# Optimization experiments

Hardware: AMD Instinct MI355X
Metric: run time of the kernel (lower is better)

## Reference

```python
import jax, jax.numpy as jnp
import numpy as np

EMB = 1024
HEADS = 16
HEAD_DIM = EMB // HEADS


def setup_inputs() -> dict:
    key = jax.random.key(0)
    ks = jax.random.split(key, 9)
    s = 1.0 / np.sqrt(EMB)
    x = jax.random.normal(ks[0], (2, 2048, EMB), dtype=jnp.float32)
    Wq = jax.random.normal(ks[1], (EMB, EMB), dtype=jnp.float32) * s
    bq = jnp.zeros((EMB,), dtype=jnp.float32)
    Wk = jax.random.normal(ks[2], (EMB, EMB), dtype=jnp.float32) * s
    bk = jnp.zeros((EMB,), dtype=jnp.float32)
    Wv = jax.random.normal(ks[3], (EMB, EMB), dtype=jnp.float32) * s
    bv = jnp.zeros((EMB,), dtype=jnp.float32)
    Wo = jax.random.normal(ks[4], (EMB, EMB), dtype=jnp.float32) * s
    bo = jnp.zeros((EMB,), dtype=jnp.float32)
    return {"x": x, "Wq": Wq, "bq": bq, "Wk": Wk, "bk": bk,
            "Wv": Wv, "bv": bv, "Wo": Wo, "bo": bo}


def reference(x, Wq, bq, Wk, bk, Wv, bv, Wo, bo):
    B, S, E = x.shape
    # torch Linear: y = x @ W.T + b
    q = x @ Wq.T + bq
    k = x @ Wk.T + bk
    v = x @ Wv.T + bv
    # [B,S,E] -> [B,H,S,D]
    q = q.reshape(B, S, HEADS, HEAD_DIM).transpose(0, 2, 1, 3)
    k = k.reshape(B, S, HEADS, HEAD_DIM).transpose(0, 2, 1, 3)
    v = v.reshape(B, S, HEADS, HEAD_DIM).transpose(0, 2, 1, 3)
    energy = jnp.einsum('bhqd,bhkd->bhqk', q, k)
    scaling = jnp.float32(E) ** 0.5  # NOTE: sqrt(emb_size), not sqrt(head_dim), as in source
    att = jax.nn.softmax(energy / scaling, axis=-1)
    out = jnp.einsum('bhqk,bhkd->bhqd', att, v)
    out = out.transpose(0, 2, 1, 3).reshape(B, S, E)
    return out @ Wo.T + bo
```

## Files before the change

### kernel.cpp

```cpp
#include <hip/hip_runtime.h>
#include <stdint.h>


typedef _Float16 half8  __attribute__((ext_vector_type(8)));
typedef _Float16 half4v __attribute__((ext_vector_type(4)));
typedef float    f32x4  __attribute__((ext_vector_type(4)));
typedef float    f32x16 __attribute__((ext_vector_type(16)));

#define GLD16(g, l) __builtin_amdgcn_global_load_lds(                         \
    (__attribute__((address_space(1))) void*)(g),                            \
    (__attribute__((address_space(3))) void*)(l), 16, 0, 0)

#define MFMA16(a, b, c) __builtin_amdgcn_mfma_f32_16x16x32_f16((a), (b), (c), 0, 0, 0)
#define MFMA32(a, b, c) __builtin_amdgcn_mfma_f32_32x32x16_f16((a), (b), (c), 0, 0, 0)

#if __has_builtin(__builtin_amdgcn_exp2f)
#define EXP2(x) __builtin_amdgcn_exp2f(x)
#else
#define EXP2(x) exp2f(x)
#endif

static __device__ inline uint32_t pk_u32(float a, float b)
{
    auto t = __builtin_amdgcn_cvt_pkrtz(a, b);
    return __builtin_bit_cast(uint32_t, t);
}

__global__ void cvt_all(const float* __restrict__ x,  const float* __restrict__ wq,
                        const float* __restrict__ wk, const float* __restrict__ wv,
                        const float* __restrict__ wo, _Float16* __restrict__ xb,
                        _Float16* __restrict__ wqkv, _Float16* __restrict__ wob)
{
    int i = blockIdx.x * blockDim.x + threadIdx.x;
    const float* src; _Float16* dst; int off;
    if (i < 1048576)      { src = x;  dst = xb;                 off = i; }
    else if (i < 1310720) { src = wq; dst = wqkv;               off = i - 1048576; }
    else if (i < 1572864) { src = wk; dst = wqkv + 1048576;     off = i - 1310720; }
    else if (i < 1835008) { src = wv; dst = wqkv + 2097152;     off = i - 1572864; }
    else                  { src = wo; dst = wob;                off = i - 1835008; }
    float4 f = ((const float4*)src)[off];
    half4v h = { (_Float16)f.x, (_Float16)f.y, (_Float16)f.z, (_Float16)f.w };
    ((half4v*)dst)[off] = h;
}

template<int BN, int MODE>
__global__ __launch_bounds__(256, MODE == 0 ? 3 : 2)
void gemm_f16(const _Float16* __restrict__ A, const _Float16* __restrict__ W,
              const float* __restrict__ b0, const float* __restrict__ b1,
              const float* __restrict__ b2, _Float16* __restrict__ o0,
              _Float16* __restrict__ o1, _Float16* __restrict__ o2,
              float* __restrict__ outf, float qscale)
{
    constexpr int NI = BN / 32;
    __shared__ _Float16 lA[128 * 64];
    __shared__ _Float16 lB[BN * 64];
    const int m0 = blockIdx.y * 128, n0 = blockIdx.x * BN;
    const int tid = threadIdx.x, lane = tid & 63, w = tid >> 6;
    const int wr = (w >> 1) * 64, wc = (w & 1) * (BN / 2);
    const int lrow = lane & 15, lk4 = lane >> 4;
    f32x4 acc[4][NI] = {};

    for (int k0 = 0; k0 < 1024; k0 += 64) {
        __syncthreads();
#pragma unroll
        for (int c = 0; c < 4; ++c) {
            int sidx = c * 256 + tid;
            int row = sidx >> 3, sl = sidx & 7;
            int gc = k0 + ((sl ^ (row & 7)) << 3);
            GLD16(A + (size_t)(m0 + row) * 1024 + gc, lA + (size_t)(c * 256 + w * 64) * 8);
        }
#pragma unroll
        for (int c = 0; c < BN / 32; ++c) {
            int sidx = c * 256 + tid;
            int row = sidx >> 3, sl = sidx & 7;
            int gc = k0 + ((sl ^ (row & 7)) << 3);
            GLD16(W + (size_t)(n0 + row) * 1024 + gc, lB + (size_t)(c * 256 + w * 64) * 8);
        }
        __syncthreads();

#pragma unroll
        for (int kd = 0; kd < 2; ++kd) {
            half8 af[4], bf[NI];
#pragma unroll
            for (int mi = 0; mi < 4; ++mi) {
                int ra = wr + mi * 16 + lrow;
                af[mi] = *(const half8*)(lA + ra * 64 + (((kd * 4 + lk4) ^ (ra & 7)) * 8));
            }
#pragma unroll
            for (int ni = 0; ni < NI; ++ni) {
                int rb = wc + ni * 16 + lrow;
                bf[ni] = *(const half8*)(lB + rb * 64 + (((kd * 4 + lk4) ^ (rb & 7)) * 8));
            }
#pragma unroll
            for (int mi = 0; mi < 4; ++mi)
#pragma unroll
                for (int ni = 0; ni < NI; ++ni)
                    acc[mi][ni] = MFMA16(af[mi], bf[ni], acc[mi][ni]);
        }
    }

    if (MODE == 0) {
        const int which = n0 >> 10;
        const float* bp = which == 0 ? b0 : which == 1 ? b1 : b2;
        const float scale = which == 0 ? qscale : 1.f;
        const int nh = n0 & 1023;
        float bcol[NI];
#pragma unroll
        for (int ni = 0; ni < NI; ++ni) bcol[ni] = bp[nh + wc + ni * 16 + lrow];
        if (which == 2) {
#pragma unroll
            for (int mi = 0; mi < 4; ++mi)
#pragma unroll
                for (int ni = 0; ni < NI; ++ni) {
                    int cg = nh + wc + ni * 16 + lrow;
                    int hh = cg >> 6, dd = cg & 63;
                    int sb = m0 + wr + mi * 16 + lk4 * 4;
                    int bb = sb >> 11, ss = sb & 2047;
                    int tile = ss >> 6, ks = (ss >> 4) & 3;
                    int hb = (ss >> 3) & 1, j0 = ss & 7;
                    int c2 = dd >> 5, l31v = dd & 31;
                    half4v pkv;
#pragma unroll
                    for (int r = 0; r < 4; ++r)
                        pkv[r] = (_Float16)(acc[mi][ni][r] + bcol[ni]);
                    size_t off = (size_t)(bb * 16 + hh) * 131072
                               + tile * 4096 + (ks * 2 + c2) * 512
                               + hb * 256 + l31v * 8 + j0;
                    *(half4v*)(o2 + off) = pkv;
                }
        } else {
            _Float16* outh = which == 0 ? o0 : o1;
#pragma unroll
            for (int mi = 0; mi < 4; ++mi)
#pragma unroll
                for (int ni = 0; ni < NI; ++ni)
#pragma unroll
                    for (int r = 0; r < 4; ++r) {
                        int rg = m0 + wr + mi * 16 + lk4 * 4 + r;
                        int cg = nh + wc + ni * 16 + lrow;
                        float v = (acc[mi][ni][r] + bcol[ni]) * scale;
                        int b = rg >> 11, s = rg & 2047, hh = cg >> 6, dd = cg & 63;
                        outh[(((size_t)b * 16 + hh) * 2048 + s) * 64 + dd] = (_Float16)v;
                    }
        }
    } else {
        float bcol[NI];
#pragma unroll
        for (int ni = 0; ni < NI; ++ni) bcol[ni] = b0[n0 + wc + ni * 16 + lrow];
#pragma unroll
        for (int mi = 0; mi < 4; ++mi)
#pragma unroll
            for (int ni = 0; ni < NI; ++ni)
#pragma unroll
                for (int r = 0; r < 4; ++r) {
                    int rg = m0 + wr + mi * 16 + lk4 * 4 + r;
                    int cg = n0 + wc + ni * 16 + lrow;
                    outf[(size_t)rg * 1024 + cg] = acc[mi][ni][r] + bcol[ni];
                }
    }
}

#define KVB 64
#define NT  32
__global__ __launch_bounds__(256, 2)
void attn(const _Float16* __restrict__ q, const _Float16* __restrict__ k,
          const _Float16* __restrict__ vtf, _Float16* __restrict__ ao)
{
    __shared__ _Float16 lKf[3 * KVB * 64];
    const int bid0 = blockIdx.x;
    const int bid = (bid0 & 7) * 64 + (bid0 >> 3);
    const int bh = bid >> 4, q0 = (bid & 15) * 128;
    const int bb = bh >> 4, hh = bh & 15;
    const int tid = threadIdx.x, lane = tid & 63, w = tid >> 6;
    const int l31 = lane & 31, h = lane >> 5;
    const int kbase = (l31 & 7) + 2 * (l31 >> 3);
    const _Float16* qh = q + (size_t)bh * 2048 * 64;
    const _Float16* kh = k + (size_t)bh * 2048 * 64;
    const _Float16* vth = vtf + (size_t)bh * 131072;

    half8 qf[4];
#pragma unroll
    for (int kd = 0; kd < 4; ++kd)
        qf[kd] = *(const half8*)(qh + (size_t)(q0 + w * 32 + l31) * 64
                                    + kd * 16 + h * 8);

    float l_ = 0.f;
    f32x16 o0 = {}, o1 = {};
    half8 vfA[8], vfB[8];

    auto STAGEK = [&](int t, int bs) {
        const int s0 = t * KVB;
        _Float16* Kd = lKf + bs * (KVB * 64);
#pragma unroll
        for (int c = 0; c < 2; ++c) {
            int p = c * 256 + tid;
            int r = p >> 3, jj = p & 7;
            int col = (jj - (r & 7) - 2 * (r >> 3)) & 7;
            GLD16(kh + (size_t)(s0 + r) * 64 + col * 8, Kd + (size_t)p * 8);
        }
    };
    auto LOADV = [&](int t, half8 (&dst)[8]) {
        const _Float16* src = vth + (size_t)t * 4096 + lane * 8;
#pragma unroll
        for (int i = 0; i < 8; ++i)
            dst[i] = *(const half8*)(src + i * 512);
    };

    STAGEK(0, 0);
    LOADV(0, vfA);
    STAGEK(1, 1);
    LOADV(1, vfB);

    auto TILE = [&](int t, int bs, half8 (&vcur)[8]) {
        if (t < NT - 1) asm volatile("s_waitcnt vmcnt(10)" ::: "memory");
        else            asm volatile("s_waitcnt vmcnt(0)" ::: "memory");
        __builtin_amdgcn_s_barrier();
        __builtin_amdgcn_sched_barrier(0);
        int bs2 = bs + 2; if (bs2 >= 3) bs2 -= 3;
        if (t + 2 < NT) STAGEK(t + 2, bs2);

        const _Float16* Kb = lKf + bs * (KVB * 64);
        half8 kf[8];
#pragma unroll
        for (int kd = 0; kd < 4; ++kd) {
            int jj = (2 * kd + h + kbase) & 7;
            kf[kd * 2]     = *(const half8*)(Kb + l31 * 64 + jj * 8);
            kf[kd * 2 + 1] = *(const half8*)(Kb + (32 + l31) * 64 + jj * 8);
        }

        f32x16 e0 = {}, e1 = {};
        __builtin_amdgcn_s_setprio(1);
#pragma unroll
        for (int kd = 0; kd < 4; ++kd) {
            e0 = MFMA32(kf[kd * 2], qf[kd], e0);
            e1 = MFMA32(kf[kd * 2 + 1], qf[kd], e1);
        }
        __builtin_amdgcn_s_setprio(0);

        half8 pa[4];
        {
            float p[16];
#pragma unroll
            for (int r = 0; r < 16; ++r) p[r] = EXP2(e0[r]);
            l_ += (((p[0] + p[1]) + (p[2] + p[3])) + ((p[4] + p[5]) + (p[6] + p[7])))
                + (((p[8] + p[9]) + (p[10] + p[11])) + ((p[12] + p[13]) + (p[14] + p[15])));
#pragma unroll
            for (int bq = 0; bq < 2; ++bq) {
                uint32_t w0 = pk_u32(p[bq * 8 + 0], p[bq * 8 + 1]);
                uint32_t w1 = pk_u32(p[bq * 8 + 2], p[bq * 8 + 3]);
                uint32_t w2 = pk_u32(p[bq * 8 + 4], p[bq * 8 + 5]);
                uint32_t w3 = pk_u32(p[bq * 8 + 6], p[bq * 8 + 7]);
                asm volatile("v_permlane32_swap_b32 %0, %1" : "+v"(w0), "+v"(w2));
                asm volatile("v_permlane32_swap_b32 %0, %1" : "+v"(w1), "+v"(w3));
                union { uint32_t u[4]; half8 hv; } uu;
                uu.u[0] = w0; uu.u[1] = w1; uu.u[2] = w2; uu.u[3] = w3;
                pa[bq] = uu.hv;
            }
        }

        __builtin_amdgcn_s_setprio(1);
        o0 = MFMA32(pa[0], vcur[0], o0);
        o1 = MFMA32(pa[0], vcur[1], o1);
        o0 = MFMA32(pa[1], vcur[2], o0);
        o1 = MFMA32(pa[1], vcur[3], o1);
        __builtin_amdgcn_s_setprio(0);

        {
            float p[16];
#pragma unroll
            for (int r = 0; r < 16; ++r) p[r] = EXP2(e1[r]);
            l_ += (((p[0] + p[1]) + (p[2] + p[3])) + ((p[4] + p[5]) + (p[6] + p[7])))
                + (((p[8] + p[9]) + (p[10] + p[11])) + ((p[12] + p[13]) + (p[14] + p[15])));
#pragma unroll
            for (int bq = 0; bq < 2; ++bq) {
                uint32_t w0 = pk_u32(p[bq * 8 + 0], p[bq * 8 + 1]);
                uint32_t w1 = pk_u32(p[bq * 8 + 2], p[bq * 8 + 3]);
                uint32_t w2 = pk_u32(p[bq * 8 + 4], p[bq * 8 + 5]);
                uint32_t w3 = pk_u32(p[bq * 8 + 6], p[bq * 8 + 7]);
                asm volatile("v_permlane32_swap_b32 %0, %1" : "+v"(w0), "+v"(w2));
                asm volatile("v_permlane32_swap_b32 %0, %1" : "+v"(w1), "+v"(w3));
                union { uint32_t u[4]; half8 hv; } uu;
                uu.u[0] = w0; uu.u[1] = w1; uu.u[2] = w2; uu.u[3] = w3;
                pa[2 + bq] = uu.hv;
            }
        }

        __builtin_amdgcn_s_setprio(1);
        o0 = MFMA32(pa[2], vcur[4], o0);
        o1 = MFMA32(pa[2], vcur[5], o1);
        o0 = MFMA32(pa[3], vcur[6], o0);
        o1 = MFMA32(pa[3], vcur[7], o1);
        __builtin_amdgcn_s_setprio(0);

        if (t + 2 < NT) LOADV(t + 2, vcur);
    };

    int cur = 0;
    for (int t = 0; t < NT; t += 2) {
        TILE(t, cur, vfA);
        int c1 = cur + 1; if (c1 >= 3) c1 -= 3;
        TILE(t + 1, c1, vfB);
        cur += 2; if (cur >= 3) cur -= 3;
    }

    l_ += __shfl_xor(l_, 32);
    const size_t obase = ((size_t)bb * 2048) * 1024 + hh * 64;
#pragma unroll
    for (int r = 0; r < 16; ++r) {
        int qr = (r & 3) + 8 * (r >> 2) + 4 * h;
        float linv = 1.f / __shfl(l_, qr);
        int sg = q0 + w * 32 + qr;
        ao[obase + (size_t)sg * 1024 + l31]      = (_Float16)(o0[r] * linv);
        ao[obase + (size_t)sg * 1024 + 32 + l31] = (_Float16)(o1[r] * linv);
    }
}

extern "C" void kernel_launch(void* const* d_in, const int* in_sizes, int n_in,
                              void* d_out, int out_size, void* d_ws, size_t ws_size,
                              hipStream_t stream)
{
    const float* x  = (const float*)d_in[0];
    const float* Wq = (const float*)d_in[1];
    const float* bq = (const float*)d_in[2];
    const float* Wk = (const float*)d_in[3];
    const float* bk = (const float*)d_in[4];
    const float* Wv = (const float*)d_in[5];
    const float* bv = (const float*)d_in[6];
    const float* Wo = (const float*)d_in[7];
    const float* bo = (const float*)d_in[8];
    float* out = (float*)d_out;

    char* ws = (char*)d_ws;
    _Float16* xb   = (_Float16*)(ws);
    _Float16* aob  = xb;
    _Float16* wqkv = (_Float16*)(ws + (8u  << 20));
    _Float16* wob  = (_Float16*)(ws + (14u << 20));
    _Float16* qb   = (_Float16*)(ws + (16u << 20));
    _Float16* kb   = (_Float16*)(ws + (24u << 20));
    _Float16* vtf  = (_Float16*)(ws + (32u << 20));

    cvt_all<<<8192, 256, 0, stream>>>(x, Wq, Wk, Wv, Wo, xb, wqkv, wob);

    const float qscale = 1.4426950408889634f / 32.f;
    gemm_f16<128, 0><<<dim3(24, 32), 256, 0, stream>>>(
        xb, wqkv, bq, bk, bv, qb, kb, vtf, nullptr, qscale);

    attn<<<512, 256, 0, stream>>>(qb, kb, vtf, aob);

    gemm_f16<64, 1><<<dim3(16, 32), 256, 0, stream>>>(
        aob, wob, bo, nullptr, nullptr, nullptr, nullptr, nullptr, out, 1.f);
}
```

Before: 109.5 us.

## Split attention KV tiles across wave pairs and pre-swizzle K into fragment layout

```diff
diff --git a/kernel.cpp b/kernel.cpp
--- a/kernel.cpp
+++ b/kernel.cpp
@@ -128,8 +128,27 @@
                                + hb * 256 + l31v * 8 + j0;
                     *(half4v*)(o2 + off) = pkv;
                 }
+        } else if (which == 1) {
+#pragma unroll
+            for (int mi = 0; mi < 4; ++mi)
+#pragma unroll
+                for (int ni = 0; ni < NI; ++ni)
+#pragma unroll
+                    for (int r = 0; r < 4; ++r) {
+                        int rg = m0 + wr + mi * 16 + lk4 * 4 + r;
+                        int cg = nh + wc + ni * 16 + lrow;
+                        float v = acc[mi][ni][r] + bcol[ni];
+                        int bb = rg >> 11, ss = rg & 2047;
+                        int hh = cg >> 6, dd = cg & 63;
+                        int tile = ss >> 6, sbl = (ss >> 5) & 1, l31v = ss & 31;
+                        int kd = dd >> 4, hv = (dd >> 3) & 1, jv = dd & 7;
+                        size_t off = (size_t)(bb * 16 + hh) * 131072
+                                   + tile * 4096 + (sbl * 4 + kd) * 512
+                                   + hv * 256 + l31v * 8 + jv;
+                        o1[off] = (_Float16)v;
+                    }
         } else {
-            _Float16* outh = which == 0 ? o0 : o1;
+            _Float16* outh = o0;
 #pragma unroll
             for (int mi = 0; mi < 4; ++mi)
 #pragma unroll
@@ -162,86 +181,77 @@
 
 #define KVB 64
 #define NT  32
-__global__ __launch_bounds__(256, 2)
-void attn(const _Float16* __restrict__ q, const _Float16* __restrict__ k,
-          const _Float16* __restrict__ vtf, _Float16* __restrict__ ao)
-{
-    __shared__ _Float16 lKf[3 * KVB * 64];
+__global__ __launch_bounds__(256, 4)
+void attn(const _Float16* __restrict__ q, const _Float16* __restrict__ kf_,
+          const _Float16* __restrict__ vf_, _Float16* __restrict__ ao)
+{
+    __shared__ _Float16 lKf[3 * 4096];
     const int bid0 = blockIdx.x;
-    const int bid = (bid0 & 7) * 64 + (bid0 >> 3);
-    const int bh = bid >> 4, q0 = (bid & 15) * 128;
+    const int bid = (bid0 & 7) * 128 + (bid0 >> 3);
+    const int bh = bid >> 5, q0 = (bid & 31) * 64;
     const int bb = bh >> 4, hh = bh & 15;
     const int tid = threadIdx.x, lane = tid & 63, w = tid >> 6;
+    const int qb = w & 1, sh = w >> 1;
     const int l31 = lane & 31, h = lane >> 5;
-    const int kbase = (l31 & 7) + 2 * (l31 >> 3);
     const _Float16* qh = q + (size_t)bh * 2048 * 64;
-    const _Float16* kh = k + (size_t)bh * 2048 * 64;
-    const _Float16* vth = vtf + (size_t)bh * 131072;
+    const _Float16* khf = kf_ + (size_t)bh * 131072;
+    const _Float16* vhf = vf_ + (size_t)bh * 131072;
 
     half8 qf[4];
 #pragma unroll
     for (int kd = 0; kd < 4; ++kd)
-        qf[kd] = *(const half8*)(qh + (size_t)(q0 + w * 32 + l31) * 64
+        qf[kd] = *(const half8*)(qh + (size_t)(q0 + qb * 32 + l31) * 64
                                     + kd * 16 + h * 8);
 
     float l_ = 0.f;
     f32x16 o0 = {}, o1 = {};
-    half8 vfA[8], vfB[8];
 
     auto STAGEK = [&](int t, int bs) {
-        const int s0 = t * KVB;
-        _Float16* Kd = lKf + bs * (KVB * 64);
+        const _Float16* src = khf + (size_t)t * 4096;
+        _Float16* dst = lKf + bs * 4096;
 #pragma unroll
         for (int c = 0; c < 2; ++c) {
             int p = c * 256 + tid;
-            int r = p >> 3, jj = p & 7;
-            int col = (jj - (r & 7) - 2 * (r >> 3)) & 7;
-            GLD16(kh + (size_t)(s0 + r) * 64 + col * 8, Kd + (size_t)p * 8);
+            GLD16(src + (size_t)p * 8, dst + (size_t)p * 8);
         }
     };
-    auto LOADV = [&](int t, half8 (&dst)[8]) {
-        const _Float16* src = vth + (size_t)t * 4096 + lane * 8;
-#pragma unroll
-        for (int i = 0; i < 8; ++i)
-            dst[i] = *(const half8*)(src + i * 512);
-    };
 
     STAGEK(0, 0);
-    LOADV(0, vfA);
     STAGEK(1, 1);
-    LOADV(1, vfB);
-
-    auto TILE = [&](int t, int bs, half8 (&vcur)[8]) {
-        if (t < NT - 1) asm volatile("s_waitcnt vmcnt(10)" ::: "memory");
-        else            asm volatile("s_waitcnt vmcnt(0)" ::: "memory");
+    asm volatile("s_waitcnt vmcnt(2)" ::: "memory");
+
+    for (int t = 0; t < NT; ++t) {
+        const int cur = t % 3;
         __builtin_amdgcn_s_barrier();
         __builtin_amdgcn_sched_barrier(0);
-        int bs2 = bs + 2; if (bs2 >= 3) bs2 -= 3;
-        if (t + 2 < NT) STAGEK(t + 2, bs2);
-
-        const _Float16* Kb = lKf + bs * (KVB * 64);
-        half8 kf[8];
-#pragma unroll
-        for (int kd = 0; kd < 4; ++kd) {
-            int jj = (2 * kd + h + kbase) & 7;
-            kf[kd * 2]     = *(const half8*)(Kb + l31 * 64 + jj * 8);
-            kf[kd * 2 + 1] = *(const half8*)(Kb + (32 + l31) * 64 + jj * 8);
-        }
-
-        f32x16 e0 = {}, e1 = {};
+
+        half8 vf[4];
+        {
+            const _Float16* src = vhf + (size_t)t * 4096 + (4 * sh) * 512 + lane * 8;
+#pragma unroll
+            for (int i = 0; i < 4; ++i)
+                vf[i] = *(const half8*)(src + i * 512);
+        }
+        if (t + 2 < NT) STAGEK(t + 2, (t + 2) % 3);
+
+        const _Float16* Kb = lKf + cur * 4096 + (sh * 4) * 512;
+        half8 kf[4];
+#pragma unroll
+        for (int kd = 0; kd < 4; ++kd)
+            kf[kd] = *(const half8*)(Kb + kd * 512 + lane * 8);
+
+        f32x16 e = {};
         __builtin_amdgcn_s_setprio(1);
 #pragma unroll
-        for (int kd = 0; kd < 4; ++kd) {
-            e0 = MFMA32(kf[kd * 2], qf[kd], e0);
-            e1 = MFMA32(kf[kd * 2 + 1], qf[kd], e1);
-        }
+        for (int kd = 0; kd < 4; ++kd)
+            e = MFMA32(kf[kd], qf[kd], e);
         __builtin_amdgcn_s_setprio(0);
 
-        half8 pa[4];
+        half8 pa[2];
         {
             float p[16];
 #pragma unroll
-            for (int r = 0; r < 16; ++r) p[r] = EXP2(e0[r]);
+            for (int r = 0; r < 16; ++r) p[r] = EXP2(e[r]);
             l_ += (((p[0] + p[1]) + (p[2] + p[3])) + ((p[4] + p[5]) + (p[6] + p[7])))
                 + (((p[8] + p[9]) + (p[10] + p[11])) + ((p[12] + p[13]) + (p[14] + p[15])));
 #pragma unroll
@@ -258,60 +268,44 @@
             }
         }
 
+        if (t + 2 < NT) asm volatile("s_waitcnt vmcnt(2)" ::: "memory");
+        else            asm volatile("s_waitcnt vmcnt(0)" ::: "memory");
+
         __builtin_amdgcn_s_setprio(1);
-        o0 = MFMA32(pa[0], vcur[0], o0);
-        o1 = MFMA32(pa[0], vcur[1], o1);
-        o0 = MFMA32(pa[1], vcur[2], o0);
-        o1 = MFMA32(pa[1], vcur[3], o1);
+        o0 = MFMA32(pa[0], vf[0], o0);
+        o1 = MFMA32(pa[0], vf[1], o1);
+        o0 = MFMA32(pa[1], vf[2], o0);
+        o1 = MFMA32(pa[1], vf[3], o1);
         __builtin_amdgcn_s_setprio(0);
-
-        {
-            float p[16];
-#pragma unroll
-            for (int r = 0; r < 16; ++r) p[r] = EXP2(e1[r]);
-            l_ += (((p[0] + p[1]) + (p[2] + p[3])) + ((p[4] + p[5]) + (p[6] + p[7])))
-                + (((p[8] + p[9]) + (p[10] + p[11])) + ((p[12] + p[13]) + (p[14] + p[15])));
-#pragma unroll
-            for (int bq = 0; bq < 2; ++bq) {
-                uint32_t w0 = pk_u32(p[bq * 8 + 0], p[bq * 8 + 1]);
-                uint32_t w1 = pk_u32(p[bq * 8 + 2], p[bq * 8 + 3]);
-                uint32_t w2 = pk_u32(p[bq * 8 + 4], p[bq * 8 + 5]);
-                uint32_t w3 = pk_u32(p[bq * 8 + 6], p[bq * 8 + 7]);
-                asm volatile("v_permlane32_swap_b32 %0, %1" : "+v"(w0), "+v"(w2));
-                asm volatile("v_permlane32_swap_b32 %0, %1" : "+v"(w1), "+v"(w3));
-                union { uint32_t u[4]; half8 hv; } uu;
-                uu.u[0] = w0; uu.u[1] = w1; uu.u[2] = w2; uu.u[3] = w3;
-                pa[2 + bq] = uu.hv;
-            }
-        }
-
-        __builtin_amdgcn_s_setprio(1);
-        o0 = MFMA32(pa[2], vcur[4], o0);
-        o1 = MFMA32(pa[2], vcur[5], o1);
-        o0 = MFMA32(pa[3], vcur[6], o0);
-        o1 = MFMA32(pa[3], vcur[7], o1);
-        __builtin_amdgcn_s_setprio(0);
-
-        if (t + 2 < NT) LOADV(t + 2, vcur);
-    };
-
-    int cur = 0;
-    for (int t = 0; t < NT; t += 2) {
-        TILE(t, cur, vfA);
-        int c1 = cur + 1; if (c1 >= 3) c1 -= 3;
-        TILE(t + 1, c1, vfB);
-        cur += 2; if (cur >= 3) cur -= 3;
     }
 
     l_ += __shfl_xor(l_, 32);
-    const size_t obase = ((size_t)bb * 2048) * 1024 + hh * 64;
-#pragma unroll
-    for (int r = 0; r < 16; ++r) {
-        int qr = (r & 3) + 8 * (r >> 2) + 4 * h;
-        float linv = 1.f / __shfl(l_, qr);
-        int sg = q0 + w * 32 + qr;
-        ao[obase + (size_t)sg * 1024 + l31]      = (_Float16)(o0[r] * linv);
-        ao[obase + (size_t)sg * 1024 + 32 + l31] = (_Float16)(o1[r] * linv);
+    __syncthreads();
+    float* mO = (float*)lKf;
+    float* mL = mO + 4096;
+    if (sh == 1) {
+#pragma unroll
+        for (int r = 0; r < 16; ++r) {
+            int qr = (r & 3) + 8 * (r >> 2) + 4 * h;
+            mO[qb * 2048 + qr * 64 + l31]      = o0[r];
+            mO[qb * 2048 + qr * 64 + 32 + l31] = o1[r];
+        }
+        if (h == 0) mL[qb * 32 + l31] = l_;
+    }
+    __syncthreads();
+    if (sh == 0) {
+        float ltot = l_ + mL[qb * 32 + l31];
+        const size_t obase = ((size_t)bb * 2048) * 1024 + hh * 64;
+#pragma unroll
+        for (int r = 0; r < 16; ++r) {
+            int qr = (r & 3) + 8 * (r >> 2) + 4 * h;
+            float linv = 1.f / __shfl(ltot, qr);
+            float v0 = o0[r] + mO[qb * 2048 + qr * 64 + l31];
+            float v1 = o1[r] + mO[qb * 2048 + qr * 64 + 32 + l31];
+            int sg = q0 + qb * 32 + qr;
+            ao[obase + (size_t)sg * 1024 + l31]      = (_Float16)(v0 * linv);
+            ao[obase + (size_t)sg * 1024 + 32 + l31] = (_Float16)(v1 * linv);
+        }
     }
 }
 
@@ -336,16 +330,16 @@
     _Float16* wqkv = (_Float16*)(ws + (8u  << 20));
     _Float16* wob  = (_Float16*)(ws + (14u << 20));
     _Float16* qb   = (_Float16*)(ws + (16u << 20));
-    _Float16* kb   = (_Float16*)(ws + (24u << 20));
-    _Float16* vtf  = (_Float16*)(ws + (32u << 20));
+    _Float16* kfb  = (_Float16*)(ws + (24u << 20));
+    _Float16* vfb  = (_Float16*)(ws + (32u << 20));
 
     cvt_all<<<8192, 256, 0, stream>>>(x, Wq, Wk, Wv, Wo, xb, wqkv, wob);
 
     const float qscale = 1.4426950408889634f / 32.f;
     gemm_f16<128, 0><<<dim3(24, 32), 256, 0, stream>>>(
-        xb, wqkv, bq, bk, bv, qb, kb, vtf, nullptr, qscale);
-
-    attn<<<512, 256, 0, stream>>>(qb, kb, vtf, aob);
+        xb, wqkv, bq, bk, bv, qb, kfb, vfb, nullptr, qscale);
+
+    attn<<<1024, 256, 0, stream>>>(qb, kfb, vfb, aob);
 
     gemm_f16<64, 1><<<dim3(16, 32), 256, 0, stream>>>(
         aob, wob, bo, nullptr, nullptr, nullptr, nullptr, nullptr, out, 1.f);
```

New measurement: 112.4 us. +2.7%, slower.
